# Kernel optimization log

Hardware: AMD Instinct MI355X
Metric: run time of the kernel (lower is better)

Reference implementation:

```python
import jax, jax.numpy as jnp
import numpy as np
from jax import lax

EPS = 1e-4  # scn BatchNorm default eps


def _subconv(x, mask, W):
    # Submanifold conv: inactive sites contribute zero, outputs only at active sites.
    x = x * mask[..., None]
    y = lax.conv_general_dilated(x, W, (1, 1), 'SAME',
                                 dimension_numbers=('NHWC', 'HWIO', 'NHWC'))
    return y * mask[..., None]


def _bnrelu(x, mask, gamma, beta):
    # BatchNormReLU over active sites only (training-mode batch stats).
    m = mask[..., None].astype(x.dtype)
    cnt = jnp.maximum(jnp.sum(m), 1.0)
    mean = jnp.sum(x * m, axis=(0, 1, 2)) / cnt
    var = jnp.sum(((x - mean) ** 2) * m, axis=(0, 1, 2)) / cnt
    y = (x - mean) * lax.rsqrt(var + EPS) * gamma + beta
    return jnp.maximum(y, 0.0) * m


def _maxpool(x, mask):
    # scn.MaxPooling(2, 3, 2): max over ACTIVE sites in each 3x3 window, stride 2.
    neg = jnp.where(mask[..., None], x, -1e30)
    y = lax.reduce_window(neg, -jnp.inf, lax.max, (1, 3, 3, 1), (1, 2, 2, 1), 'VALID')
    mf = lax.reduce_window(mask.astype(x.dtype), 0.0, lax.max, (1, 3, 3), (1, 2, 2), 'VALID')
    mnew = mf > 0
    return jnp.where(mnew[..., None], y, 0.0), mnew


def _gru(x, h, mask, Wg, Wc):
    # Sparse ConvGRU: gates via submanifold convs on concat(x, h).
    g = jax.nn.sigmoid(_subconv(jnp.concatenate([x, h], -1), mask, Wg))
    u, r = jnp.split(g, 2, axis=-1)
    c = jnp.tanh(_subconv(jnp.concatenate([x, r * h], -1), mask, Wc))
    return (h * (1.0 - u) + c * u) * mask[..., None]


def setup_inputs() -> dict:
    key = jax.random.key(0)
    ks = jax.random.split(key, 32)
    B, H, W0, Cin = 32, 191, 255, 2
    mask = jax.random.uniform(ks[0], (B, H, W0)) < 0.1
    x = jax.random.normal(ks[1], (B, H, W0, Cin), jnp.float32) * mask[..., None]

    def w(k, shape, fan_in):
        return (jax.random.normal(k, shape, jnp.float32) / np.sqrt(fan_in)).astype(jnp.float32)

    inp = {'x': x, 'mask': mask}
    chans = [(2, 16), (16, 32), (32, 64), (64, 128), (128, 256)]
    i = 2
    for li, (ci, co) in enumerate(chans, 1):
        inp['c%da' % li] = w(ks[i], (3, 3, ci, co), 9 * ci); i += 1
        inp['bn%dg' % li] = jnp.ones((co,), jnp.float32)
        inp['bn%db' % li] = jnp.zeros((co,), jnp.float32)
        inp['c%db' % li] = w(ks[i], (3, 3, co, co), 9 * co); i += 1
    C = 256
    inp['g1Wg'] = w(ks[i], (3, 3, 2 * C, 2 * C), 18 * C); i += 1
    inp['g1Wc'] = w(ks[i], (3, 3, 2 * C, C), 18 * C); i += 1
    inp['g2Wg'] = w(ks[i], (3, 3, 2 * C, 2 * C), 18 * C); i += 1
    inp['g2Wc'] = w(ks[i], (3, 3, 2 * C, C), 18 * C); i += 1
    nr_classes, nr_box = 2, 2
    feat = 5 * 7 * 256  # linear_input_features
    inp['W1'] = w(ks[i], (feat, 1024), feat); i += 1
    inp['b1'] = jnp.zeros((1024,), jnp.float32)
    odim = 5 * 7 * (nr_classes + 5 * nr_box)
    inp['W2'] = w(ks[i], (1024, odim), 1024); i += 1
    inp['b2'] = jnp.zeros((odim,), jnp.float32)
    return inp


def reference(x, mask, c1a, bn1g, bn1b, c1b, c2a, bn2g, bn2b, c2b,
              c3a, bn3g, bn3b, c3b, c4a, bn4g, bn4b, c4b,
              c5a, bn5g, bn5b, c5b, g1Wg, g1Wc, g2Wg, g2Wc, W1, b1, W2, b2):
    levels = [(c1a, bn1g, bn1b, c1b), (c2a, bn2g, bn2b, c2b),
              (c3a, bn3g, bn3b, c3b), (c4a, bn4g, bn4b, c4b),
              (c5a, bn5g, bn5b, c5b)]
    h, m = x, mask
    for ca, g, b, cb in levels:  # fixed 5-block backbone (all appended to conv1)
        h = _subconv(h, m, ca)
        h = _bnrelu(h, m, g, b)
        h = _subconv(h, m, cb)
        h, m = _maxpool(h, m)
    # prev_states is None -> zero hidden states
    h1 = _gru(h, jnp.zeros_like(h), m, g1Wg, g1Wc)
    h2 = _gru(h1, jnp.zeros_like(h1), m, g2Wg, g2Wc)
    B = x.shape[0]
    # SparseToDense yields NCHW in torch; flatten in that order before the MLP head
    dense = jnp.transpose(h2, (0, 3, 1, 2)).reshape(B, -1)  # [B, 256*5*7]
    y = jnp.maximum(dense @ W1 + b1, 0.0)
    y = y @ W2 + b2
    out = y.reshape(B, 5, 7, -1)  # [B, 5, 7, nr_classes + 5*nr_box]
    return out, h1, h2
```

## Files before the change

### kernel.cpp

```cpp
#include <hip/hip_runtime.h>
#include <stdint.h>

#define TPB 256

typedef _Float16 half_t;
typedef __attribute__((ext_vector_type(8))) _Float16 f16x8;
typedef __attribute__((ext_vector_type(4))) float f32x4;

static inline int nblk(long n) { return (int)((n + TPB - 1) / TPB); }

__global__ void cmpA0_k(const float* __restrict__ x, int n, int* __restrict__ bcnt) {
  int i = blockIdx.x * TPB + threadIdx.x;
  bool a = false;
  if (i < n) {
    float2 v = *(const float2*)(x + 2L * i);
    a = (v.x != 0.f) || (v.y != 0.f);
  }
  unsigned long long bal = __ballot(a);
  __shared__ int wc[4];
  if ((threadIdx.x & 63) == 0) wc[threadIdx.x >> 6] = __popcll(bal);
  __syncthreads();
  if (threadIdx.x == 0) bcnt[blockIdx.x] = wc[0] + wc[1] + wc[2] + wc[3];
}

__global__ void cmpB0_k(const float* __restrict__ x, int n, const int* __restrict__ bbase,
                        int* __restrict__ list, int* __restrict__ inv, int cap,
                        half_t* __restrict__ xh) {
  int i = blockIdx.x * TPB + threadIdx.x;
  float2 v = {0.f, 0.f};
  bool a = false;
  if (i < n) {
    v = *(const float2*)(x + 2L * i);
    a = (v.x != 0.f) || (v.y != 0.f);
  }
  unsigned long long bal = __ballot(a);
  __shared__ int wc[4];
  int wid = threadIdx.x >> 6, lane = threadIdx.x & 63;
  if (lane == 0) wc[wid] = __popcll(bal);
  __syncthreads();
  int base = bbase[blockIdx.x];
  for (int w = 0; w < wid; ++w) base += wc[w];
  if (i < n) {
    xh[2L * i] = (half_t)v.x;
    xh[2L * i + 1] = (half_t)v.y;
    int pos = base + __popcll(bal & ((1ull << lane) - 1));
    if (a && pos < cap) { list[pos] = i; inv[i] = pos; }
    else inv[i] = -1;
  }
}

__device__ __forceinline__ bool actp(const int* invp, int Hp, int Wp, int Ho, int Wo, int i) {
  int wo = i % Wo; int t = i / Wo; int ho = t % Ho; int bb = t / Ho;
  long rb = ((long)bb * Hp + 2 * ho) * Wp + 2 * wo;
  bool a = false;
  #pragma unroll
  for (int kh = 0; kh < 3; ++kh)
    #pragma unroll
    for (int kw = 0; kw < 3; ++kw)
      a |= (invp[rb + kh * Wp + kw] >= 0);
  return a;
}

__global__ void poolA_k(const int* __restrict__ invp, int Hp, int Wp, int Ho, int Wo,
                        int n, int* __restrict__ bcnt, uint8_t* __restrict__ actm) {
  int i = blockIdx.x * TPB + threadIdx.x;
  bool a = (i < n) && actp(invp, Hp, Wp, Ho, Wo, i);
  if (i < n) actm[i] = (uint8_t)a;
  unsigned long long bal = __ballot(a);
  __shared__ int wc[4];
  if ((threadIdx.x & 63) == 0) wc[threadIdx.x >> 6] = __popcll(bal);
  __syncthreads();
  if (threadIdx.x == 0) bcnt[blockIdx.x] = wc[0] + wc[1] + wc[2] + wc[3];
}

__global__ void poolB_k(const uint8_t* __restrict__ actm, int n,
                        const int* __restrict__ bbase, int* __restrict__ list,
                        int* __restrict__ inv, int cap) {
  int i = blockIdx.x * TPB + threadIdx.x;
  bool a = (i < n) && (actm[i] != 0);
  unsigned long long bal = __ballot(a);
  __shared__ int wc[4];
  int wid = threadIdx.x >> 6, lane = threadIdx.x & 63;
  if (lane == 0) wc[wid] = __popcll(bal);
  __syncthreads();
  int base = bbase[blockIdx.x];
  for (int w = 0; w < wid; ++w) base += wc[w];
  if (i < n) {
    int pos = base + __popcll(bal & ((1ull << lane) - 1));
    if (a && pos < cap) { list[pos] = i; inv[i] = pos; }
    else inv[i] = -1;
  }
}

__global__ void scan_k(int* __restrict__ b, int n, int* __restrict__ total,
                       float* __restrict__ stats) {
  __shared__ int sh[1024];
  __shared__ int sc;
  if (threadIdx.x < 512) stats[threadIdx.x] = 0.f;
  if (threadIdx.x == 0) sc = 0;
  __syncthreads();
  for (int base = 0; base < n; base += 1024) {
    int i = base + threadIdx.x;
    int v = (i < n) ? b[i] : 0;
    sh[threadIdx.x] = v;
    __syncthreads();
    for (int o = 1; o < 1024; o <<= 1) {
      int t = (threadIdx.x >= o) ? sh[threadIdx.x - o] : 0;
      __syncthreads();
      sh[threadIdx.x] += t;
      __syncthreads();
    }
    if (i < n) b[i] = sh[threadIdx.x] - v + sc;
    __syncthreads();
    if (threadIdx.x == 0) sc += sh[1023];
    __syncthreads();
  }
  if (threadIdx.x == 0) *total = sc;
}

template <int C>
__global__ void pool_val_f16_k(const half_t* __restrict__ xin, const int* __restrict__ invp,
                               const int* __restrict__ list, const int* __restrict__ cnt,
                               int Hp, int Wp, int Ho, int Wo, half_t* __restrict__ y) {
  constexpr int CV = C / 8;
  long total = (long)cnt[0] * CV;
  for (long i = (long)blockIdx.x * TPB + threadIdx.x; i < total; i += (long)gridDim.x * TPB) {
    int cb = (int)(i & (CV - 1));
    int r = (int)(i / CV);
    int site = list[r];
    int wo = site % Wo; int t = site / Wo; int ho = t % Ho; int bb = t / Ho;
    long rb = ((long)bb * Hp + 2 * ho) * Wp + 2 * wo;
    float best[8];
    #pragma unroll
    for (int z = 0; z < 8; ++z) best[z] = -1e30f;
    #pragma unroll
    for (int kh = 0; kh < 3; ++kh)
      #pragma unroll
      for (int kw = 0; kw < 3; ++kw) {
        int j = invp[rb + kh * Wp + kw];
        if (j >= 0) {
          f16x8 v = *(const f16x8*)(xin + (long)j * C + cb * 8);
          #pragma unroll
          for (int z = 0; z < 8; ++z) best[z] = fmaxf(best[z], (float)v[z]);
        }
      }
    f16x8 o;
    #pragma unroll
    for (int z = 0; z < 8; ++z) o[z] = (half_t)best[z];
    *(f16x8*)(y + (long)r * C + cb * 8) = o;
  }
}

struct PackArgs {
  const float* src[14];
  half_t* dst[14];
  const float* W1;
  half_t* w1t;
  float* h1;
  float* h2;
  half_t* df;
};

__global__ void megaprep_k(PackArgs pa) {
  __shared__ float tile[64][65];
  const int seg = blockIdx.y;
  const int tci[14]  = {2, 16, 16, 32, 32, 64, 64, 128, 128, 256, 256, 256, 256, 256};
  const int tco[14]  = {16, 16, 32, 32, 64, 64, 128, 128, 256, 256, 256, 256, 256, 256};
  const int tkp[14]  = {32, 160, 160, 288, 0, 0, 0, 0, 0, 0, 0, 0, 0, 0};
  const int twci[14] = {2, 16, 16, 32, 32, 64, 64, 128, 128, 256, 512, 512, 512, 512};
  const int twco[14] = {16, 16, 32, 32, 64, 64, 128, 128, 256, 256, 512, 256, 512, 256};
  if (seg < 5) {
    const int CI = tci[seg], CO = tco[seg], KP = tkp[seg];
    const int wci = twci[seg], wco = twco[seg];
    const float* __restrict__ src = pa.src[seg];
    half_t* __restrict__ dst = pa.dst[seg];
    if (KP > 0) {
      long total = (long)CO * KP;
      for (long i = (long)blockIdx.x * TPB + threadIdx.x; i < total; i += (long)gridDim.x * TPB) {
        int k = (int)(i % KP), co = (int)(i / KP);
        int tap = k / CI, ci = k - tap * CI;
        float v = (tap < 9) ? src[((long)tap * wci + ci) * wco + co] : 0.f;
        dst[i] = (half_t)v;
      }
    } else {
      long total = 9L * CO * CI;
      for (long i = (long)blockIdx.x * TPB + threadIdx.x; i < total; i += (long)gridDim.x * TPB) {
        int ci = (int)(i % CI);
        long t = i / CI;
        int co = (int)(t % CO);
        int tap = (int)(t / CO);
        dst[i] = (half_t)src[((long)tap * wci + ci) * wco + co];
      }
    }
  } else if (seg < 14) {
    const int CI = tci[seg], CO = tco[seg];
    const int wci = twci[seg], wco = twco[seg];
    const int cit_n = CI >> 6, cot_n = CO >> 6;
    const int ntiles = 9 * cit_n * cot_n;
    int bx = blockIdx.x;
    if (bx >= ntiles) return;
    int tap = bx / (cit_n * cot_n);
    int rem = bx - tap * (cit_n * cot_n);
    int cit = rem / cot_n, cot = rem - cit * cot_n;
    const float* __restrict__ src = pa.src[seg];
    half_t* __restrict__ dst = pa.dst[seg];
    const long sbase = ((long)tap * wci + cit * 64) * wco + cot * 64;
    for (int i = threadIdx.x; i < 1024; i += TPB) {
      int r = i >> 4, c4 = i & 15;
      float4 v = *(const float4*)(src + sbase + (long)r * wco + c4 * 4);
      tile[r][c4 * 4 + 0] = v.x;
      tile[r][c4 * 4 + 1] = v.y;
      tile[r][c4 * 4 + 2] = v.z;
      tile[r][c4 * 4 + 3] = v.w;
    }
    __syncthreads();
    const long dbase = ((long)tap * CO + cot * 64) * CI + cit * 64;
    for (int i = threadIdx.x; i < 512; i += TPB) {
      int r = i >> 3, c8 = i & 7;
      f16x8 o;
      #pragma unroll
      for (int z = 0; z < 8; ++z) o[z] = (half_t)tile[c8 * 8 + z][r];
      *(f16x8*)(dst + dbase + (long)r * CI + c8 * 8) = o;
    }
  } else if (seg == 14) {
    for (long i = (long)blockIdx.x * TPB + threadIdx.x; i < 286720; i += (long)gridDim.x * TPB) {
      pa.h1[i] = 0.f;
      pa.h2[i] = 0.f;
      pa.df[i] = (half_t)0.f;
    }
  } else {
    int bx = blockIdx.x;
    if (bx >= 2240) return;
    int k0 = (bx >> 4) * 64, j0 = (bx & 15) * 64;
    for (int i = threadIdx.x; i < 1024; i += TPB) {
      int r = i >> 4, c4 = i & 15;
      float4 v = *(const float4*)(pa.W1 + (long)(k0 + r) * 1024 + j0 + c4 * 4);
      tile[r][c4 * 4 + 0] = v.x;
      tile[r][c4 * 4 + 1] = v.y;
      tile[r][c4 * 4 + 2] = v.z;
      tile[r][c4 * 4 + 3] = v.w;
    }
    __syncthreads();
    for (int i = threadIdx.x; i < 512; i += TPB) {
      int r = i >> 3, c8 = i & 7;
      f16x8 o;
      #pragma unroll
      for (int z = 0; z < 8; ++z) o[z] = (half_t)tile[c8 * 8 + z][r];
      *(f16x8*)(pa.w1t + (long)(j0 + r) * 8960 + k0 + c8 * 8) = o;
    }
  }
}

template <int CI, int CO, bool DENSE>
__global__ __launch_bounds__(256) void mconvp_k(const half_t* __restrict__ X,
                                                const half_t* __restrict__ Wt,
                                                half_t* __restrict__ y,
                                                const int* __restrict__ inv,
                                                const int* __restrict__ list,
                                                const int* __restrict__ cnt,
                                                int H, int W) {
  constexpr int KP = ((9 * CI + 31) / 32) * 32;
  constexpr int NCO = CO / 16;
  const int nact = cnt[0];
  const int base = blockIdx.x * 64;
  if (base >= nact) return;
  __shared__ int nbr[64 * 9];
  for (int i = threadIdx.x; i < 64 * 9; i += TPB) {
    int s = i / 9, nb = i - s * 9;
    int j = -1;
    if (base + s < nact) {
      int site = list[base + s];
      int w = site % W; int t = site / W; int h = t % H; int bb = t / H;
      int hh = h + nb / 3 - 1, ww = w + nb % 3 - 1;
      if ((unsigned)hh < (unsigned)H && (unsigned)ww < (unsigned)W) {
        int ss = (bb * H + hh) * W + ww;
        j = DENSE ? ss : inv[ss];
      }
    }
    nbr[i] = j;
  }
  __syncthreads();
  const int lane = threadIdx.x & 63, wv = threadIdx.x >> 6;
  const int srow = lane & 15, kseg = lane >> 4;
  const int sloc = wv * 16 + srow;
  f32x4 acc[NCO];
  #pragma unroll
  for (int c = 0; c < NCO; ++c) acc[c] = (f32x4){0.f, 0.f, 0.f, 0.f};
  #pragma unroll
  for (int k0 = 0; k0 < KP; k0 += 32) {
    const int k = k0 + kseg * 8;
    f16x8 av;
    #pragma unroll
    for (int z = 0; z < 8; ++z) av[z] = (_Float16)0.f;
    if (CI >= 8) {
      int tap = k / CI;
      int ci = k - tap * CI;
      if (tap < 9) {
        int j = nbr[sloc * 9 + tap];
        if (j >= 0) av = *(const f16x8*)(X + (long)j * CI + ci);
      }
    } else {
      #pragma unroll
      for (int q = 0; q < 4; ++q) {
        int kk = k + 2 * q;
        int tap = kk >> 1;
        if (tap < 9) {
          int j = nbr[sloc * 9 + tap];
          if (j >= 0) {
            const half_t* xp = X + (long)j * 2;
            av[2 * q] = xp[0];
            av[2 * q + 1] = xp[1];
          }
        }
      }
    }
    #pragma unroll
    for (int c = 0; c < NCO; ++c) {
      f16x8 bv = *(const f16x8*)(Wt + (long)(c * 16 + srow) * KP + k);
      acc[c] = __builtin_amdgcn_mfma_f32_16x16x32_f16(av, bv, acc[c], 0, 0, 0);
    }
  }
  #pragma unroll
  for (int c = 0; c < NCO; ++c)
    #pragma unroll
    for (int r = 0; r < 4; ++r) {
      int ss = base + wv * 16 + kseg * 4 + r;
      if (ss < nact) y[(long)ss * CO + c * 16 + srow] = (half_t)acc[c][r];
    }
}

template <int CI>
__global__ __launch_bounds__(256) void mconv_lds_k(const half_t* __restrict__ X,
                                                   const half_t* __restrict__ Wt,
                                                   half_t* __restrict__ y,
                                                   const int* __restrict__ inv,
                                                   const int* __restrict__ list,
                                                   const int* __restrict__ cnt,
                                                   int H, int W, int COfull) {
  constexpr int NK = CI / 32;
  constexpr int LDW = CI + 8;
  __shared__ half_t wlds[64 * LDW];
  const int nact = cnt[0];
  const int base = blockIdx.x * 64;
  if (base >= nact) return;
  const int lane = threadIdx.x & 63, wv = threadIdx.x >> 6;
  const int srow = lane & 15, kseg = lane >> 4;
  const int co0 = blockIdx.y * 64;
  int jj[9];
  {
    int s = base + wv * 16 + srow;
    bool sv = (s < nact);
    int h = 0, w = 0, bb = 0;
    if (sv) {
      int site = list[s];
      w = site % W;
      int t = site / W;
      h = t % H;
      bb = t / H;
    }
    #pragma unroll
    for (int tap = 0; tap < 9; ++tap) {
      int j = -1;
      if (sv) {
        int hh = h + tap / 3 - 1, ww = w + tap % 3 - 1;
        if ((unsigned)hh < (unsigned)H && (unsigned)ww < (unsigned)W)
          j = inv[(bb * H + hh) * W + ww];
      }
      jj[tap] = j;
    }
  }
  f32x4 acc[4];
  #pragma unroll
  for (int b = 0; b < 4; ++b) acc[b] = (f32x4){0.f, 0.f, 0.f, 0.f};
  for (int tap = 0; tap < 9; ++tap) {
    __syncthreads();
    constexpr int GR = 64 * (CI / 8);
    const half_t* wsrc = Wt + ((long)tap * COfull + co0) * CI;
    for (int idx = threadIdx.x; idx < GR; idx += TPB) {
      int row = idx / (CI / 8), cb = idx % (CI / 8);
      *(f16x8*)(&wlds[row * LDW + cb * 8]) = *(const f16x8*)(wsrc + (long)row * CI + cb * 8);
    }
    __syncthreads();
    const int j = jj[tap];
    f16x8 av[NK];
    #pragma unroll
    for (int s = 0; s < NK; ++s) {
      #pragma unroll
      for (int z = 0; z < 8; ++z) av[s][z] = (_Float16)0.f;
      if (j >= 0) av[s] = *(const f16x8*)(X + (long)j * CI + kseg * 8 + s * 32);
    }
    #pragma unroll
    for (int s = 0; s < NK; ++s) {
      #pragma unroll
      for (int b = 0; b < 4; ++b) {
        f16x8 bv = *(const f16x8*)(&wlds[(b * 16 + srow) * LDW + kseg * 8 + s * 32]);
        acc[b] = __builtin_amdgcn_mfma_f32_16x16x32_f16(av[s], bv, acc[b], 0, 0, 0);
      }
    }
  }
  #pragma unroll
  for (int b = 0; b < 4; ++b)
    #pragma unroll
    for (int r = 0; r < 4; ++r) {
      int ss = base + wv * 16 + kseg * 4 + r;
      if (ss < nact) y[(long)ss * COfull + co0 + b * 16 + srow] = (half_t)acc[b][r];
    }
}

template <int CI>
__global__ __launch_bounds__(256) void gruconv16_k(const half_t* __restrict__ X,
                                                   const half_t* __restrict__ Wg,
                                                   const half_t* __restrict__ Wc,
                                                   float* __restrict__ hdense,
                                                   half_t* __restrict__ hcomp,
                                                   half_t* __restrict__ dflat,
                                                   const int* __restrict__ inv,
                                                   const int* __restrict__ list,
                                                   const int* __restrict__ cnt,
                                                   int H, int W) {
  constexpr int CO = 256;
  constexpr int NK = CI / 32;
  const int nact = cnt[0];
  const int base = blockIdx.x * 16;
  if (base >= nact) return;
  __shared__ int nbr[16 * 9];
  __shared__ float red[4][16][34];
  for (int i = threadIdx.x; i < 16 * 9; i += TPB) {
    int s = i / 9, nb = i - s * 9;
    int j = -1;
    if (base + s < nact) {
      int site = list[base + s];
      int w = site % W; int t = site / W; int h = t % H; int bb = t / H;
      int hh = h + nb / 3 - 1, ww = w + nb % 3 - 1;
      if ((unsigned)hh < (unsigned)H && (unsigned)ww < (unsigned)W)
        j = inv[(bb * H + hh) * W + ww];
    }
    nbr[i] = j;
  }
  __syncthreads();
  const int lane = threadIdx.x & 63, wv = threadIdx.x >> 6;
  const int srow = lane & 15, kseg = lane >> 4;
  const int co0 = blockIdx.y * 16;
  const int t0 = (wv * 9) / 4, t1 = ((wv + 1) * 9) / 4;
  f32x4 g = {0.f, 0.f, 0.f, 0.f};
  f32x4 c = g;
  for (int tap = t0; tap < t1; ++tap) {
    int j = nbr[srow * 9 + tap];
    const half_t* xp = X + (long)j * CI + kseg * 8;
    const half_t* wgp = Wg + ((long)tap * CO + co0 + srow) * CI + kseg * 8;
    const half_t* wcp = Wc + ((long)tap * CO + co0 + srow) * CI + kseg * 8;
    f16x8 av[NK];
    #pragma unroll
    for (int s = 0; s < NK; ++s) {
      #pragma unroll
      for (int z = 0; z < 8; ++z) av[s][z] = (_Float16)0.f;
      if (j >= 0) av[s] = *(const f16x8*)(xp + s * 32);
    }
    #pragma unroll
    for (int s = 0; s < NK; ++s) {
      f16x8 bg = *(const f16x8*)(wgp + s * 32);
      f16x8 bc = *(const f16x8*)(wcp + s * 32);
      g = __builtin_amdgcn_mfma_f32_16x16x32_f16(av[s], bg, g, 0, 0, 0);
      c = __builtin_amdgcn_mfma_f32_16x16x32_f16(av[s], bc, c, 0, 0, 0);
    }
  }
  #pragma unroll
  for (int r = 0; r < 4; ++r) {
    int s = kseg * 4 + r;
    red[wv][s][srow] = g[r];
    red[wv][s][16 + srow] = c[r];
  }
  __syncthreads();
  {
    int i = threadIdx.x;
    int s = i >> 4, co = i & 15;
    float gs = red[0][s][co] + red[1][s][co] + red[2][s][co] + red[3][s][co];
    float cs = red[0][s][16 + co] + red[1][s][16 + co] + red[2][s][16 + co] + red[3][s][16 + co];
    int ss = base + s;
    if (ss < nact) {
      float u = 1.f / (1.f + expf(-gs));
      float v = u * tanhf(cs);
      if (hcomp) hcomp[(long)ss * CO + co0 + co] = (half_t)v;
      int site = list[ss];
      hdense[(long)site * CO + co0 + co] = v;
      if (dflat) {
        int b = site / 35, s2 = site - b * 35;
        dflat[(long)b * 8960 + (co0 + co) * 35 + s2] = (half_t)v;
      }
    }
  }
}

template <int CO>
__global__ void bn_stats2_k(const half_t* __restrict__ y, const int* __restrict__ cnt,
                            float* __restrict__ stats) {
  __shared__ float ls[512];
  for (int i = threadIdx.x; i < 2 * CO; i += TPB) ls[i] = 0.f;
  __syncthreads();
  long total = (long)cnt[0] * CO;
  long i0 = (long)blockIdx.x * TPB + threadIdx.x;
  int c = (int)(i0 & (CO - 1));
  float s = 0.f, s2 = 0.f;
  for (long i = i0; i < total; i += (long)gridDim.x * TPB) {
    float v = (float)y[i];
    s += v; s2 += v * v;
  }
  atomicAdd(&ls[c], s);
  atomicAdd(&ls[CO + c], s2);
  __syncthreads();
  for (int i = threadIdx.x; i < 2 * CO; i += TPB) atomicAdd(&stats[i], ls[i]);
}

template <int C>
__global__ void bnapply_f16_k(const half_t* __restrict__ y, const int* __restrict__ cnt,
                              const float* __restrict__ stats, const float* __restrict__ gamma,
                              const float* __restrict__ beta, half_t* __restrict__ out) {
  __shared__ float sc[C], sh2[C];
  for (int c = threadIdx.x; c < C; c += TPB) {
    float n = fmaxf((float)cnt[0], 1.f);
    float mean = stats[c] / n;
    float var = fmaxf(stats[C + c] / n - mean * mean, 0.f);
    float s = gamma[c] * rsqrtf(var + 1e-4f);
    sc[c] = s;
    sh2[c] = beta[c] - mean * s;
  }
  __syncthreads();
  long total = (long)cnt[0] * C;
  for (long i = (long)blockIdx.x * TPB + threadIdx.x; i < total; i += (long)gridDim.x * TPB) {
    int c = (int)(i & (C - 1));
    out[i] = (half_t)fmaxf(fmaf((float)y[i], sc[c], sh2[c]), 0.f);
  }
}

#define KS1 35
__global__ __launch_bounds__(256) void lin1m_k(const half_t* __restrict__ D,
                                               const half_t* __restrict__ W1T,
                                               float* __restrict__ part) {
  __shared__ float red[4][32][65];
  const int lane = threadIdx.x & 63, wv = threadIdx.x >> 6;
  const int srow = lane & 15, kseg = lane >> 4;
  const int kc = blockIdx.x, j0 = blockIdx.y * 64;
  const int kbase = kc * 256 + wv * 64;
  f32x4 acc[2][4];
  #pragma unroll
  for (int m = 0; m < 2; ++m)
    #pragma unroll
    for (int b = 0; b < 4; ++b) acc[m][b] = (f32x4){0.f, 0.f, 0.f, 0.f};
  #pragma unroll
  for (int step = 0; step < 2; ++step) {
    int k = kbase + step * 32 + kseg * 8;
    f16x8 a0 = *(const f16x8*)(D + (long)srow * 8960 + k);
    f16x8 a1 = *(const f16x8*)(D + (long)(16 + srow) * 8960 + k);
    #pragma unroll
    for (int b = 0; b < 4; ++b) {
      f16x8 bv = *(const f16x8*)(W1T + (long)(j0 + b * 16 + srow) * 8960 + k);
      acc[0][b] = __builtin_amdgcn_mfma_f32_16x16x32_f16(a0, bv, acc[0][b], 0, 0, 0);
      acc[1][b] = __builtin_amdgcn_mfma_f32_16x16x32_f16(a1, bv, acc[1][b], 0, 0, 0);
    }
  }
  #pragma unroll
  for (int m = 0; m < 2; ++m)
    #pragma unroll
    for (int b = 0; b < 4; ++b)
      #pragma unroll
      for (int r = 0; r < 4; ++r)
        red[wv][m * 16 + kseg * 4 + r][b * 16 + srow] = acc[m][b][r];
  __syncthreads();
  for (int i = threadIdx.x; i < 32 * 64; i += TPB) {
    int row = i >> 6, col = i & 63;
    float v = red[0][row][col] + red[1][row][col] + red[2][row][col] + red[3][row][col];
    part[(long)kc * 32768 + row * 1024 + j0 + col] = v;
  }
}

__global__ void lin1_reduce_k(const float* __restrict__ part, const float* __restrict__ b1,
                              float* __restrict__ y1) {
  int i = blockIdx.x * TPB + threadIdx.x;
  if (i >= 32 * 1024) return;
  int b = i >> 10, j = i & 1023;
  float a = b1[j];
  #pragma unroll
  for (int kc = 0; kc < KS1; ++kc) a += part[(long)kc * 32768 + b * 1024 + j];
  y1[i] = fmaxf(a, 0.f);
}

#define JS2 8
__global__ void lin2_part_k(const float* __restrict__ y1, const float* __restrict__ W2,
                            float* __restrict__ part2) {
  int i = blockIdx.x * TPB + threadIdx.x;
  if (i >= 32 * 420) return;
  int b = i / 420, o = i - b * 420;
  int j0 = blockIdx.y * 128;
  float a = 0.f;
  const float* yp = y1 + b * 1024 + j0;
  const float* wp = W2 + (long)j0 * 420 + o;
  #pragma unroll 8
  for (int j = 0; j < 128; ++j) a = fmaf(yp[j], wp[(long)j * 420], a);
  part2[(long)blockIdx.y * 13440 + i] = a;
}

__global__ void lin2_fin_k(const float* __restrict__ part2, const float* __restrict__ b2,
                           float* __restrict__ out) {
  int i = blockIdx.x * TPB + threadIdx.x;
  if (i >= 32 * 420) return;
  int o = i % 420;
  float a = b2[o];
  #pragma unroll
  for (int js = 0; js < JS2; ++js) a += part2[(long)js * 13440 + i];
  out[i] = a;
}

extern "C" void kernel_launch(void* const* d_in, const int* in_sizes, int n_in,
                              void* d_out, int out_size, void* d_ws, size_t ws_size,
                              hipStream_t stream) {
  const float* x = (const float*)d_in[0];
  const float* ca[5] = {(const float*)d_in[2], (const float*)d_in[6], (const float*)d_in[10],
                        (const float*)d_in[14], (const float*)d_in[18]};
  const float* bg[5] = {(const float*)d_in[3], (const float*)d_in[7], (const float*)d_in[11],
                        (const float*)d_in[15], (const float*)d_in[19]};
  const float* bb[5] = {(const float*)d_in[4], (const float*)d_in[8], (const float*)d_in[12],
                        (const float*)d_in[16], (const float*)d_in[20]};
  const float* cb[5] = {(const float*)d_in[5], (const float*)d_in[9], (const float*)d_in[13],
                        (const float*)d_in[17], (const float*)d_in[21]};
  const float* g1Wg = (const float*)d_in[22];
  const float* g1Wc = (const float*)d_in[23];
  const float* g2Wg = (const float*)d_in[24];
  const float* g2Wc = (const float*)d_in[25];
  const float* W1 = (const float*)d_in[26];
  const float* b1 = (const float*)d_in[27];
  const float* W2 = (const float*)d_in[28];
  const float* b2 = (const float*)d_in[29];

  const int Hs[6] = {191, 95, 47, 23, 11, 5};
  const int Wd[6] = {255, 127, 63, 31, 15, 7};
  const long NS[6] = {1558560, 386080, 94752, 22816, 5280, 1120};
  const int cap[6] = {160000, 386080, 94752, 22816, 5280, 1120};

  float* ws = (float*)d_ws;
  long off = 0;
  float* part = ws + off;  off += 1200000;
  float* part2 = ws + off; off += 120000;
  float* stats = ws + off; off += 512;
  float* y1 = ws + off;    off += 32L * 1024;

  half_t* hbase = (half_t*)(ws + off);
  long hoff = 0;
  half_t* hbufA = hbase + hoff; hoff += 6500000;
  half_t* hbufB = hbase + hoff; hoff += 6500000;
  half_t* hbufC = hbase + hoff; hoff += 6500000;
  half_t* xh = hbase + hoff;    hoff += 3117120;
  half_t* w1t = hbase + hoff;   hoff += 9175040;
  half_t* df16 = hbase + hoff;  hoff += 286720;
  half_t* wp_ca0 = hbase + hoff; hoff += 16L * 32;
  half_t* wp_cb0 = hbase + hoff; hoff += 16L * 160;
  half_t* wp_ca1 = hbase + hoff; hoff += 32L * 160;
  half_t* wp_cb1 = hbase + hoff; hoff += 32L * 288;
  half_t* wt_ca2 = hbase + hoff; hoff += 9L * 64 * 32;
  half_t* wt_cb2 = hbase + hoff; hoff += 9L * 64 * 64;
  half_t* wt_ca3 = hbase + hoff; hoff += 9L * 128 * 64;
  half_t* wt_cb3 = hbase + hoff; hoff += 9L * 128 * 128;
  half_t* wt_ca4 = hbase + hoff; hoff += 9L * 256 * 128;
  half_t* wt_cb4 = hbase + hoff; hoff += 9L * 256 * 256;
  half_t* wt_g1g = hbase + hoff; hoff += 9L * 256 * 256;
  half_t* wt_g1c = hbase + hoff; hoff += 9L * 256 * 256;
  half_t* wt_g2g = hbase + hoff; hoff += 9L * 256 * 256;
  half_t* wt_g2c = hbase + hoff; hoff += 9L * 256 * 256;

  int* ip = (int*)(hbase + hoff);
  long ioff = 0;
  int* cnt = ip + ioff; ioff += 16;
  int* bcnt = ip + ioff; ioff += 8192;
  int* list[6]; int* inv[6];
  for (int l = 0; l < 6; ++l) { list[l] = ip + ioff; ioff += cap[l]; }
  for (int l = 0; l < 6; ++l) { inv[l] = ip + ioff; ioff += NS[l]; }
  uint8_t* actm = (uint8_t*)(ip + ioff);
  long aoff = NS[1];
  size_t needed = (size_t)off * 4 + (size_t)hoff * 2 + (size_t)ioff * 4 + (size_t)aoff;
  if (ws_size < needed) return;

  float* h1d = (float*)d_out + 13440;
  float* h2d = h1d + 286720;

  PackArgs pa;
  pa.src[0] = ca[0]; pa.dst[0] = wp_ca0;
  pa.src[1] = cb[0]; pa.dst[1] = wp_cb0;
  pa.src[2] = ca[1]; pa.dst[2] = wp_ca1;
  pa.src[3] = cb[1]; pa.dst[3] = wp_cb1;
  pa.src[4] = ca[2]; pa.dst[4] = wt_ca2;
  pa.src[5] = cb[2]; pa.dst[5] = wt_cb2;
  pa.src[6] = ca[3]; pa.dst[6] = wt_ca3;
  pa.src[7] = cb[3]; pa.dst[7] = wt_cb3;
  pa.src[8] = ca[4]; pa.dst[8] = wt_ca4;
  pa.src[9] = cb[4]; pa.dst[9] = wt_cb4;
  pa.src[10] = g1Wg; pa.dst[10] = wt_g1g;
  pa.src[11] = g1Wc; pa.dst[11] = wt_g1c;
  pa.src[12] = g2Wg; pa.dst[12] = wt_g2g;
  pa.src[13] = g2Wc; pa.dst[13] = wt_g2c;
  pa.W1 = W1; pa.w1t = w1t;
  pa.h1 = h1d; pa.h2 = h2d; pa.df = df16;
  megaprep_k<<<dim3(2240, 16), TPB, 0, stream>>>(pa);

  {
    int nb = nblk(NS[0]);
    cmpA0_k<<<nb, TPB, 0, stream>>>(x, (int)NS[0], bcnt);
    scan_k<<<1, 1024, 0, stream>>>(bcnt, nb, cnt + 0, stats);
    cmpB0_k<<<nb, TPB, 0, stream>>>(x, (int)NS[0], bcnt, list[0], inv[0], cap[0], xh);
  }

  mconvp_k<2, 16, true><<<(cap[0] + 63) / 64, TPB, 0, stream>>>(
      xh, wp_ca0, hbufC, nullptr, list[0], cnt + 0, Hs[0], Wd[0]);
  bn_stats2_k<16><<<288, TPB, 0, stream>>>(hbufC, cnt + 0, stats);
  bnapply_f16_k<16><<<2048, TPB, 0, stream>>>(hbufC, cnt + 0, stats, bg[0], bb[0], hbufA);
  mconvp_k<16, 16, false><<<(cap[0] + 63) / 64, TPB, 0, stream>>>(
      hbufA, wp_cb0, hbufC, inv[0], list[0], cnt + 0, Hs[0], Wd[0]);
  {
    int nb = nblk(NS[1]);
    poolA_k<<<nb, TPB, 0, stream>>>(inv[0], Hs[0], Wd[0], Hs[1], Wd[1], (int)NS[1], bcnt, actm);
    scan_k<<<1, 1024, 0, stream>>>(bcnt, nb, cnt + 1, stats);
    poolB_k<<<nb, TPB, 0, stream>>>(actm, (int)NS[1], bcnt, list[1], inv[1], cap[1]);
  }
  pool_val_f16_k<16><<<1024, TPB, 0, stream>>>(hbufC, inv[0], list[1], cnt + 1, Hs[0], Wd[0], Hs[1], Wd[1], hbufB);

  mconvp_k<16, 32, false><<<(cap[1] + 63) / 64, TPB, 0, stream>>>(
      hbufB, wp_ca1, hbufC, inv[1], list[1], cnt + 1, Hs[1], Wd[1]);
  bn_stats2_k<32><<<288, TPB, 0, stream>>>(hbufC, cnt + 1, stats);
  bnapply_f16_k<32><<<2048, TPB, 0, stream>>>(hbufC, cnt + 1, stats, bg[1], bb[1], hbufA);
  mconvp_k<32, 32, false><<<(cap[1] + 63) / 64, TPB, 0, stream>>>(
      hbufA, wp_cb1, hbufC, inv[1], list[1], cnt + 1, Hs[1], Wd[1]);
  {
    int nb = nblk(NS[2]);
    poolA_k<<<nb, TPB, 0, stream>>>(inv[1], Hs[1], Wd[1], Hs[2], Wd[2], (int)NS[2], bcnt, actm);
    scan_k<<<1, 1024, 0, stream>>>(bcnt, nb, cnt + 2, stats);
    poolB_k<<<nb, TPB, 0, stream>>>(actm, (int)NS[2], bcnt, list[2], inv[2], cap[2]);
  }
  pool_val_f16_k<32><<<1024, TPB, 0, stream>>>(hbufC, inv[1], list[2], cnt + 2, Hs[1], Wd[1], Hs[2], Wd[2], hbufB);

  mconv_lds_k<32><<<dim3((cap[2] + 63) / 64, 1), TPB, 0, stream>>>(
      hbufB, wt_ca2, hbufC, inv[2], list[2], cnt + 2, Hs[2], Wd[2], 64);
  bn_stats2_k<64><<<288, TPB, 0, stream>>>(hbufC, cnt + 2, stats);
  bnapply_f16_k<64><<<2048, TPB, 0, stream>>>(hbufC, cnt + 2, stats, bg[2], bb[2], hbufA);
  mconv_lds_k<64><<<dim3((cap[2] + 63) / 64, 1), TPB, 0, stream>>>(
      hbufA, wt_cb2, hbufC, inv[2], list[2], cnt + 2, Hs[2], Wd[2], 64);
  {
    int nb = nblk(NS[3]);
    poolA_k<<<nb, TPB, 0, stream>>>(inv[2], Hs[2], Wd[2], Hs[3], Wd[3], (int)NS[3], bcnt, actm);
    scan_k<<<1, 1024, 0, stream>>>(bcnt, nb, cnt + 3, stats);
    poolB_k<<<nb, TPB, 0, stream>>>(actm, (int)NS[3], bcnt, list[3], inv[3], cap[3]);
  }
  pool_val_f16_k<64><<<1024, TPB, 0, stream>>>(hbufC, inv[2], list[3], cnt + 3, Hs[2], Wd[2], Hs[3], Wd[3], hbufB);

  mconv_lds_k<64><<<dim3((cap[3] + 63) / 64, 2), TPB, 0, stream>>>(
      hbufB, wt_ca3, hbufC, inv[3], list[3], cnt + 3, Hs[3], Wd[3], 128);
  bn_stats2_k<128><<<288, TPB, 0, stream>>>(hbufC, cnt + 3, stats);
  bnapply_f16_k<128><<<2048, TPB, 0, stream>>>(hbufC, cnt + 3, stats, bg[3], bb[3], hbufA);
  mconv_lds_k<128><<<dim3((cap[3] + 63) / 64, 2), TPB, 0, stream>>>(
      hbufA, wt_cb3, hbufC, inv[3], list[3], cnt + 3, Hs[3], Wd[3], 128);
  {
    int nb = nblk(NS[4]);
    poolA_k<<<nb, TPB, 0, stream>>>(inv[3], Hs[3], Wd[3], Hs[4], Wd[4], (int)NS[4], bcnt, actm);
    scan_k<<<1, 1024, 0, stream>>>(bcnt, nb, cnt + 4, stats);
    poolB_k<<<nb, TPB, 0, stream>>>(actm, (int)NS[4], bcnt, list[4], inv[4], cap[4]);
  }
  pool_val_f16_k<128><<<1024, TPB, 0, stream>>>(hbufC, inv[3], list[4], cnt + 4, Hs[3], Wd[3], Hs[4], Wd[4], hbufB);

  mconv_lds_k<128><<<dim3((cap[4] + 63) / 64, 4), TPB, 0, stream>>>(
      hbufB, wt_ca4, hbufC, inv[4], list[4], cnt + 4, Hs[4], Wd[4], 256);
  bn_stats2_k<256><<<288, TPB, 0, stream>>>(hbufC, cnt + 4, stats);
  bnapply_f16_k<256><<<2048, TPB, 0, stream>>>(hbufC, cnt + 4, stats, bg[4], bb[4], hbufA);
  mconv_lds_k<256><<<dim3((cap[4] + 63) / 64, 4), TPB, 0, stream>>>(
      hbufA, wt_cb4, hbufC, inv[4], list[4], cnt + 4, Hs[4], Wd[4], 256);
  {
    int nb = nblk(NS[5]);
    poolA_k<<<nb, TPB, 0, stream>>>(inv[4], Hs[4], Wd[4], Hs[5], Wd[5], (int)NS[5], bcnt, actm);
    scan_k<<<1, 1024, 0, stream>>>(bcnt, nb, cnt + 5, stats);
    poolB_k<<<nb, TPB, 0, stream>>>(actm, (int)NS[5], bcnt, list[5], inv[5], cap[5]);
  }
  pool_val_f16_k<256><<<1024, TPB, 0, stream>>>(hbufC, inv[4], list[5], cnt + 5, Hs[4], Wd[4], Hs[5], Wd[5], hbufB);

  gruconv16_k<256><<<dim3((cap[5] + 15) / 16, 16), TPB, 0, stream>>>(
      hbufB, wt_g1g, wt_g1c, h1d, hbufA, nullptr, inv[5], list[5], cnt + 5, Hs[5], Wd[5]);
  gruconv16_k<256><<<dim3((cap[5] + 15) / 16, 16), TPB, 0, stream>>>(
      hbufA, wt_g2g, wt_g2c, h2d, nullptr, df16, inv[5], list[5], cnt + 5, Hs[5], Wd[5]);

  lin1m_k<<<dim3(KS1, 16), TPB, 0, stream>>>(df16, w1t, part);
  lin1_reduce_k<<<nblk(32L * 1024), TPB, 0, stream>>>(part, b1, y1);
  lin2_part_k<<<dim3(nblk(32L * 420), JS2), TPB, 0, stream>>>(y1, W2, part2);
  lin2_fin_k<<<nblk(32L * 420), TPB, 0, stream>>>(part2, b2, (float*)d_out);
}
```

Before: 560.5 us.

## Replace three-kernel stream compaction with single-pass decoupled look-back scan

```diff
diff --git a/kernel.cpp b/kernel.cpp
--- a/kernel.cpp
+++ b/kernel.cpp
@@ -6,48 +6,9 @@
 typedef _Float16 half_t;
 typedef __attribute__((ext_vector_type(8))) _Float16 f16x8;
 typedef __attribute__((ext_vector_type(4))) float f32x4;
+typedef unsigned long long ull;
 
 static inline int nblk(long n) { return (int)((n + TPB - 1) / TPB); }
-
-__global__ void cmpA0_k(const float* __restrict__ x, int n, int* __restrict__ bcnt) {
-  int i = blockIdx.x * TPB + threadIdx.x;
-  bool a = false;
-  if (i < n) {
-    float2 v = *(const float2*)(x + 2L * i);
-    a = (v.x != 0.f) || (v.y != 0.f);
-  }
-  unsigned long long bal = __ballot(a);
-  __shared__ int wc[4];
-  if ((threadIdx.x & 63) == 0) wc[threadIdx.x >> 6] = __popcll(bal);
-  __syncthreads();
-  if (threadIdx.x == 0) bcnt[blockIdx.x] = wc[0] + wc[1] + wc[2] + wc[3];
-}
-
-__global__ void cmpB0_k(const float* __restrict__ x, int n, const int* __restrict__ bbase,
-                        int* __restrict__ list, int* __restrict__ inv, int cap,
-                        half_t* __restrict__ xh) {
-  int i = blockIdx.x * TPB + threadIdx.x;
-  float2 v = {0.f, 0.f};
-  bool a = false;
-  if (i < n) {
-    v = *(const float2*)(x + 2L * i);
-    a = (v.x != 0.f) || (v.y != 0.f);
-  }
-  unsigned long long bal = __ballot(a);
-  __shared__ int wc[4];
-  int wid = threadIdx.x >> 6, lane = threadIdx.x & 63;
-  if (lane == 0) wc[wid] = __popcll(bal);
-  __syncthreads();
-  int base = bbase[blockIdx.x];
-  for (int w = 0; w < wid; ++w) base += wc[w];
-  if (i < n) {
-    xh[2L * i] = (half_t)v.x;
-    xh[2L * i + 1] = (half_t)v.y;
-    int pos = base + __popcll(bal & ((1ull << lane) - 1));
-    if (a && pos < cap) { list[pos] = i; inv[i] = pos; }
-    else inv[i] = -1;
-  }
-}
 
 __device__ __forceinline__ bool actp(const int* invp, int Hp, int Wp, int Ho, int Wo, int i) {
   int wo = i % Wo; int t = i / Wo; int ho = t % Ho; int bb = t / Ho;
@@ -61,61 +22,58 @@
   return a;
 }
 
-__global__ void poolA_k(const int* __restrict__ invp, int Hp, int Wp, int Ho, int Wo,
-                        int n, int* __restrict__ bcnt, uint8_t* __restrict__ actm) {
+template <bool L0>
+__global__ void cscan_k(const float* __restrict__ x, const int* __restrict__ invp,
+                        int Hp, int Wp, int Ho, int Wo, int n,
+                        ull* __restrict__ state, int* __restrict__ list,
+                        int* __restrict__ inv, int cap, int* __restrict__ total,
+                        float* __restrict__ stats, half_t* __restrict__ xh) {
   int i = blockIdx.x * TPB + threadIdx.x;
-  bool a = (i < n) && actp(invp, Hp, Wp, Ho, Wo, i);
-  if (i < n) actm[i] = (uint8_t)a;
+  bool a = false;
+  if (i < n) {
+    if (L0) {
+      float2 v = *(const float2*)(x + 2L * i);
+      a = (v.x != 0.f) || (v.y != 0.f);
+      xh[2L * i] = (half_t)v.x;
+      xh[2L * i + 1] = (half_t)v.y;
+    } else {
+      a = actp(invp, Hp, Wp, Ho, Wo, i);
+    }
+  }
   unsigned long long bal = __ballot(a);
   __shared__ int wc[4];
-  if ((threadIdx.x & 63) == 0) wc[threadIdx.x >> 6] = __popcll(bal);
-  __syncthreads();
-  if (threadIdx.x == 0) bcnt[blockIdx.x] = wc[0] + wc[1] + wc[2] + wc[3];
-}
-
-__global__ void poolB_k(const uint8_t* __restrict__ actm, int n,
-                        const int* __restrict__ bbase, int* __restrict__ list,
-                        int* __restrict__ inv, int cap) {
-  int i = blockIdx.x * TPB + threadIdx.x;
-  bool a = (i < n) && (actm[i] != 0);
-  unsigned long long bal = __ballot(a);
-  __shared__ int wc[4];
+  __shared__ int s_excl;
   int wid = threadIdx.x >> 6, lane = threadIdx.x & 63;
   if (lane == 0) wc[wid] = __popcll(bal);
   __syncthreads();
-  int base = bbase[blockIdx.x];
-  for (int w = 0; w < wid; ++w) base += wc[w];
+  if (threadIdx.x == 0) {
+    int agg = wc[0] + wc[1] + wc[2] + wc[3];
+    atomicExch(&state[blockIdx.x], (1ull << 32) | (unsigned)agg);
+    long ex = 0;
+    int pred = (int)blockIdx.x - 1;
+    while (pred >= 0) {
+      ull st;
+      do { st = atomicAdd(&state[pred], 0ull); } while ((st >> 32) == 0);
+      ex += (int)(st & 0xffffffffu);
+      if ((st >> 32) == 2u) break;
+      --pred;
+    }
+    atomicExch(&state[blockIdx.x], (2ull << 32) | (unsigned)(ex + agg));
+    s_excl = (int)ex;
+    if (blockIdx.x == gridDim.x - 1) *total = (int)(ex + agg);
+  }
+  if (blockIdx.x == 0) {
+    stats[threadIdx.x] = 0.f;
+    stats[threadIdx.x + 256] = 0.f;
+  }
+  __syncthreads();
   if (i < n) {
+    int base = s_excl;
+    for (int w = 0; w < wid; ++w) base += wc[w];
     int pos = base + __popcll(bal & ((1ull << lane) - 1));
     if (a && pos < cap) { list[pos] = i; inv[i] = pos; }
     else inv[i] = -1;
   }
-}
-
-__global__ void scan_k(int* __restrict__ b, int n, int* __restrict__ total,
-                       float* __restrict__ stats) {
-  __shared__ int sh[1024];
-  __shared__ int sc;
-  if (threadIdx.x < 512) stats[threadIdx.x] = 0.f;
-  if (threadIdx.x == 0) sc = 0;
-  __syncthreads();
-  for (int base = 0; base < n; base += 1024) {
-    int i = base + threadIdx.x;
-    int v = (i < n) ? b[i] : 0;
-    sh[threadIdx.x] = v;
-    __syncthreads();
-    for (int o = 1; o < 1024; o <<= 1) {
-      int t = (threadIdx.x >= o) ? sh[threadIdx.x - o] : 0;
-      __syncthreads();
-      sh[threadIdx.x] += t;
-      __syncthreads();
-    }
-    if (i < n) b[i] = sh[threadIdx.x] - v + sc;
-    __syncthreads();
-    if (threadIdx.x == 0) sc += sh[1023];
-    __syncthreads();
-  }
-  if (threadIdx.x == 0) *total = sc;
 }
 
 template <int C>
@@ -159,6 +117,7 @@
   float* h1;
   float* h2;
   half_t* df;
+  ull* state;
 };
 
 __global__ void megaprep_k(PackArgs pa) {
@@ -228,6 +187,8 @@
       pa.h2[i] = 0.f;
       pa.df[i] = (half_t)0.f;
     }
+    for (long i = (long)blockIdx.x * TPB + threadIdx.x; i < 8192; i += (long)gridDim.x * TPB)
+      pa.state[i] = 0ull;
   } else {
     int bx = blockIdx.x;
     if (bx >= 2240) return;
@@ -666,17 +627,24 @@
   half_t* wt_g2g = hbase + hoff; hoff += 9L * 256 * 256;
   half_t* wt_g2c = hbase + hoff; hoff += 9L * 256 * 256;
 
-  int* ip = (int*)(hbase + hoff);
+  uintptr_t pal = (uintptr_t)(hbase + hoff);
+  pal = (pal + 7) & ~(uintptr_t)7;
+  ull* state = (ull*)pal;
+  int* ip = (int*)(state + 8192);
   long ioff = 0;
   int* cnt = ip + ioff; ioff += 16;
-  int* bcnt = ip + ioff; ioff += 8192;
   int* list[6]; int* inv[6];
   for (int l = 0; l < 6; ++l) { list[l] = ip + ioff; ioff += cap[l]; }
   for (int l = 0; l < 6; ++l) { inv[l] = ip + ioff; ioff += NS[l]; }
-  uint8_t* actm = (uint8_t*)(ip + ioff);
-  long aoff = NS[1];
-  size_t needed = (size_t)off * 4 + (size_t)hoff * 2 + (size_t)ioff * 4 + (size_t)aoff;
+  size_t needed = (pal - (uintptr_t)d_ws) + 8192 * 8 + (size_t)ioff * 4;
   if (ws_size < needed) return;
+
+  ull* st0 = state + 0;
+  ull* st1 = state + 6089;
+  ull* st2 = state + 7598;
+  ull* st3 = state + 7969;
+  ull* st4 = state + 8059;
+  ull* st5 = state + 8080;
 
   float* h1d = (float*)d_out + 13440;
   float* h2d = h1d + 286720;
@@ -698,14 +666,11 @@
   pa.src[13] = g2Wc; pa.dst[13] = wt_g2c;
   pa.W1 = W1; pa.w1t = w1t;
   pa.h1 = h1d; pa.h2 = h2d; pa.df = df16;
+  pa.state = state;
   megaprep_k<<<dim3(2240, 16), TPB, 0, stream>>>(pa);
 
-  {
-    int nb = nblk(NS[0]);
-    cmpA0_k<<<nb, TPB, 0, stream>>>(x, (int)NS[0], bcnt);
-    scan_k<<<1, 1024, 0, stream>>>(bcnt, nb, cnt + 0, stats);
-    cmpB0_k<<<nb, TPB, 0, stream>>>(x, (int)NS[0], bcnt, list[0], inv[0], cap[0], xh);
-  }
+  cscan_k<true><<<nblk(NS[0]), TPB, 0, stream>>>(
+      x, nullptr, 0, 0, 0, 0, (int)NS[0], st0, list[0], inv[0], cap[0], cnt + 0, stats, xh);
 
   mconvp_k<2, 16, true><<<(cap[0] + 63) / 64, TPB, 0, stream>>>(
       xh, wp_ca0, hbufC, nullptr, list[0], cnt + 0, Hs[0], Wd[0]);
@@ -713,12 +678,9 @@
   bnapply_f16_k<16><<<2048, TPB, 0, stream>>>(hbufC, cnt + 0, stats, bg[0], bb[0], hbufA);
   mconvp_k<16, 16, false><<<(cap[0] + 63) / 64, TPB, 0, stream>>>(
       hbufA, wp_cb0, hbufC, inv[0], list[0], cnt + 0, Hs[0], Wd[0]);
-  {
-    int nb = nblk(NS[1]);
-    poolA_k<<<nb, TPB, 0, stream>>>(inv[0], Hs[0], Wd[0], Hs[1], Wd[1], (int)NS[1], bcnt, actm);
-    scan_k<<<1, 1024, 0, stream>>>(bcnt, nb, cnt + 1, stats);
-    poolB_k<<<nb, TPB, 0, stream>>>(actm, (int)NS[1], bcnt, list[1], inv[1], cap[1]);
-  }
+  cscan_k<false><<<nblk(NS[1]), TPB, 0, stream>>>(
+      nullptr, inv[0], Hs[0], Wd[0], Hs[1], Wd[1], (int)NS[1], st1, list[1], inv[1], cap[1],
+      cnt + 1, stats, nullptr);
   pool_val_f16_k<16><<<1024, TPB, 0, stream>>>(hbufC, inv[0], list[1], cnt + 1, Hs[0], Wd[0], Hs[1], Wd[1], hbufB);
 
   mconvp_k<16, 32, false><<<(cap[1] + 63) / 64, TPB, 0, stream>>>(
@@ -727,12 +689,9 @@
   bnapply_f16_k<32><<<2048, TPB, 0, stream>>>(hbufC, cnt + 1, stats, bg[1], bb[1], hbufA);
   mconvp_k<32, 32, false><<<(cap[1] + 63) / 64, TPB, 0, stream>>>(
       hbufA, wp_cb1, hbufC, inv[1], list[1], cnt + 1, Hs[1], Wd[1]);
-  {
-    int nb = nblk(NS[2]);
-    poolA_k<<<nb, TPB, 0, stream>>>(inv[1], Hs[1], Wd[1], Hs[2], Wd[2], (int)NS[2], bcnt, actm);
-    scan_k<<<1, 1024, 0, stream>>>(bcnt, nb, cnt + 2, stats);
-    poolB_k<<<nb, TPB, 0, stream>>>(actm, (int)NS[2], bcnt, list[2], inv[2], cap[2]);
-  }
+  cscan_k<false><<<nblk(NS[2]), TPB, 0, stream>>>(
+      nullptr, inv[1], Hs[1], Wd[1], Hs[2], Wd[2], (int)NS[2], st2, list[2], inv[2], cap[2],
+      cnt + 2, stats, nullptr);
   pool_val_f16_k<32><<<1024, TPB, 0, stream>>>(hbufC, inv[1], list[2], cnt + 2, Hs[1], Wd[1], Hs[2], Wd[2], hbufB);
 
   mconv_lds_k<32><<<dim3((cap[2] + 63) / 64, 1), TPB, 0, stream>>>(
@@ -741,12 +700,9 @@
   bnapply_f16_k<64><<<2048, TPB, 0, stream>>>(hbufC, cnt + 2, stats, bg[2], bb[2], hbufA);
   mconv_lds_k<64><<<dim3((cap[2] + 63) / 64, 1), TPB, 0, stream>>>(
       hbufA, wt_cb2, hbufC, inv[2], list[2], cnt + 2, Hs[2], Wd[2], 64);
-  {
-    int nb = nblk(NS[3]);
-    poolA_k<<<nb, TPB, 0, stream>>>(inv[2], Hs[2], Wd[2], Hs[3], Wd[3], (int)NS[3], bcnt, actm);
-    scan_k<<<1, 1024, 0, stream>>>(bcnt, nb, cnt + 3, stats);
-    poolB_k<<<nb, TPB, 0, stream>>>(actm, (int)NS[3], bcnt, list[3], inv[3], cap[3]);
-  }
+  cscan_k<false><<<nblk(NS[3]), TPB, 0, stream>>>(
+      nullptr, inv[2], Hs[2], Wd[2], Hs[3], Wd[3], (int)NS[3], st3, list[3], inv[3], cap[3],
+      cnt + 3, stats, nullptr);
   pool_val_f16_k<64><<<1024, TPB, 0, stream>>>(hbufC, inv[2], list[3], cnt + 3, Hs[2], Wd[2], Hs[3], Wd[3], hbufB);
 
   mconv_lds_k<64><<<dim3((cap[3] + 63) / 64, 2), TPB, 0, stream>>>(
@@ -755,12 +711,9 @@
   bnapply_f16_k<128><<<2048, TPB, 0, stream>>>(hbufC, cnt + 3, stats, bg[3], bb[3], hbufA);
   mconv_lds_k<128><<<dim3((cap[3] + 63) / 64, 2), TPB, 0, stream>>>(
       hbufA, wt_cb3, hbufC, inv[3], list[3], cnt + 3, Hs[3], Wd[3], 128);
-  {
-    int nb = nblk(NS[4]);
-    poolA_k<<<nb, TPB, 0, stream>>>(inv[3], Hs[3], Wd[3], Hs[4], Wd[4], (int)NS[4], bcnt, actm);
-    scan_k<<<1, 1024, 0, stream>>>(bcnt, nb, cnt + 4, stats);
-    poolB_k<<<nb, TPB, 0, stream>>>(actm, (int)NS[4], bcnt, list[4], inv[4], cap[4]);
-  }
+  cscan_k<false><<<nblk(NS[4]), TPB, 0, stream>>>(
+      nullptr, inv[3], Hs[3], Wd[3], Hs[4], Wd[4], (int)NS[4], st4, list[4], inv[4], cap[4],
+      cnt + 4, stats, nullptr);
   pool_val_f16_k<128><<<1024, TPB, 0, stream>>>(hbufC, inv[3], list[4], cnt + 4, Hs[3], Wd[3], Hs[4], Wd[4], hbufB);
 
   mconv_lds_k<128><<<dim3((cap[4] + 63) / 64, 4), TPB, 0, stream>>>(
@@ -769,12 +722,9 @@
   bnapply_f16_k<256><<<2048, TPB, 0, stream>>>(hbufC, cnt + 4, stats, bg[4], bb[4], hbufA);
   mconv_lds_k<256><<<dim3((cap[4] + 63) / 64, 4), TPB, 0, stream>>>(
       hbufA, wt_cb4, hbufC, inv[4], list[4], cnt + 4, Hs[4], Wd[4], 256);
-  {
-    int nb = nblk(NS[5]);
-    poolA_k<<<nb, TPB, 0, stream>>>(inv[4], Hs[4], Wd[4], Hs[5], Wd[5], (int)NS[5], bcnt, actm);
-    scan_k<<<1, 1024, 0, stream>>>(bcnt, nb, cnt + 5, stats);
-    poolB_k<<<nb, TPB, 0, stream>>>(actm, (int)NS[5], bcnt, list[5], inv[5], cap[5]);
-  }
+  cscan_k<false><<<nblk(NS[5]), TPB, 0, stream>>>(
+      nullptr, inv[4], Hs[4], Wd[4], Hs[5], Wd[5], (int)NS[5], st5, list[5], inv[5], cap[5],
+      cnt + 5, stats, nullptr);
   pool_val_f16_k<256><<<1024, TPB, 0, stream>>>(hbufC, inv[4], list[5], cnt + 5, Hs[4], Wd[4], Hs[5], Wd[5], hbufB);
 
   gruconv16_k<256><<<dim3((cap[5] + 15) / 16, 16), TPB, 0, stream>>>(
```

New measurement: 641.3 us. 1.14x slower.
